# Kernel optimization log

Hardware: AMD Instinct MI355X
Metric: run time of the kernel (lower is better)

The kernel has to match this reference:

```python
import jax, jax.numpy as jnp
import numpy as np

B, T, D, H = 8, 1024, 512, 8
HD = D // H  # head_dim = 64


def conv1d(x, w, b):
    # x: [B, C_in, T], w: [C_out, C_in, 3], 'same' padding
    y = jax.lax.conv_general_dilated(x, w, (1,), [(1, 1)],
                                     dimension_numbers=('NCH', 'OIH', 'NCH'))
    return y + b[None, :, None]


def setup_inputs() -> dict:
    key = jax.random.key(0)
    ks = jax.random.split(key, 9)
    s = 0.05
    return {
        'x': jax.random.normal(ks[0], (B, T, D), dtype=jnp.float32),
        'w11': jax.random.normal(ks[1], (D, D, 3), dtype=jnp.float32) * s,
        'b11': jnp.zeros((D,), dtype=jnp.float32),
        'w12': jax.random.normal(ks[2], (D, D, 3), dtype=jnp.float32) * s,
        'b12': jnp.zeros((D,), dtype=jnp.float32),
        'w13': jax.random.normal(ks[3], (D, D, 3), dtype=jnp.float32) * s,
        'b13': jnp.zeros((D,), dtype=jnp.float32),
        'w2': jax.random.normal(ks[4], (D, 2 * D, 3), dtype=jnp.float32) * s,
        'b2': jnp.zeros((D,), dtype=jnp.float32),
    }


def reference(x, w11, b11, w12, b12, w13, b13, w2, b2):
    # dropout is identity in eval mode
    b, t, d = x.shape
    xc = jnp.transpose(x, (0, 2, 1))  # [B, D, T]

    def proj(w, bb):
        y = jax.nn.relu(conv1d(xc, w, bb))        # [B, D, T]
        y = jnp.transpose(y, (0, 2, 1))           # [B, T, D]
        return y.reshape(b, t, H, HD)             # [B, T, H, HD]

    q = proj(w11, b11)
    k = proj(w12, b12)
    v = proj(w13, b13)

    # ---- time-wise attention (d_k = head_dim) ----
    qf = jnp.transpose(q, (0, 2, 1, 3))  # [B, H, T, HD]
    kf = jnp.transpose(k, (0, 2, 1, 3))
    vf = jnp.transpose(v, (0, 2, 1, 3))
    sf = jnp.einsum('bhtd,bhsd->bhts', qf, kf) / np.sqrt(HD)  # [B,H,T,T]
    af = jax.nn.softmax(sf, axis=-1)
    valuesf = jnp.einsum('bhts,bhsd->bhtd', af, vf)           # [B,H,T,HD]
    valuesf = jnp.transpose(valuesf, (0, 2, 1, 3)).reshape(b, t, H * HD)

    # ---- channel-wise attention (d_k = T, scores over head_dim) ----
    qt = jnp.transpose(q, (0, 2, 3, 1))  # [B, H, HD, T]
    kt = jnp.transpose(k, (0, 2, 3, 1))
    vt = jnp.transpose(v, (0, 2, 3, 1))
    st = jnp.einsum('bhct,bhdt->bhcd', qt, kt) / np.sqrt(t)   # [B,H,HD,HD]
    at = jax.nn.softmax(st, axis=-1)
    valuest = jnp.einsum('bhcd,bhdt->bhct', at, vt)           # [B,H,HD,T]
    # torch: permute(0,2,3,1).reshape(B, T, H*HD)
    valuest = jnp.transpose(valuest, (0, 2, 3, 1)).reshape(b, t, H * HD)

    values = jnp.concatenate([valuesf, valuest], axis=-1)     # [B, T, 2D]
    values = jnp.transpose(values, (0, 2, 1))                 # [B, 2D, T]
    out = jax.nn.relu(conv1d(values, w2, b2))                 # [B, D, T]
    return jnp.transpose(out, (0, 2, 1))                      # [B, T, D]
```

## Files before the change

### kernel.cpp

```cpp
#include <hip/hip_runtime.h>

#define BB 8
#define TT 1024
#define DD 512
#define DD2 1024
#define HH 8
#define HDIM 64
#define TP (TT + 2)

typedef short short8 __attribute__((ext_vector_type(8)));
typedef float floatx4 __attribute__((ext_vector_type(4)));

typedef const __attribute__((address_space(1))) unsigned int* gas_ptr;
typedef __attribute__((address_space(3))) unsigned int* las_ptr;

__device__ __forceinline__ unsigned short f2bf(float f) {
    union { float f; unsigned u; } v; v.f = f;
    unsigned r = v.u + 0x7fffu + ((v.u >> 16) & 1u);
    return (unsigned short)(r >> 16);
}

__device__ __forceinline__ void gl2lds16(const void* g, void* l) {
    __builtin_amdgcn_global_load_lds((gas_ptr)g, (las_ptr)l, 16, 0, 0);
}

#define NX4BLK 4104
#define NW1BLK 9216
#define NW2BLK 6144
#define NZBLK 1024
__global__ void k_prep(const float* __restrict__ x, const float* __restrict__ w0,
                       const float* __restrict__ w1, const float* __restrict__ w2,
                       const float* __restrict__ wo,
                       unsigned short* __restrict__ xp, unsigned short* __restrict__ wqkv,
                       unsigned short* __restrict__ w2k, unsigned short* __restrict__ vp,
                       float* __restrict__ gbuf) {
    int blk = blockIdx.x;
    if (blk < NX4BLK) {
        int idx = blk * 256 + threadIdx.x;
        int c4 = idx % (DD / 4);
        int rt = idx / (DD / 4);
        int row = rt % TP;
        int b = rt / TP;
        ushort4 o = {0, 0, 0, 0};
        if (row >= 1 && row <= TT) {
            float4 vv = *(const float4*)&x[((size_t)(b * TT + row - 1)) * DD + c4 * 4];
            o.x = f2bf(vv.x); o.y = f2bf(vv.y); o.z = f2bf(vv.z); o.w = f2bf(vv.w);
        }
        *(ushort4*)&xp[(size_t)idx * 4] = o;
        return;
    }
    blk -= NX4BLK;
    if (blk < NW1BLK) {
        int idx = blk * 256 + threadIdx.x;
        int e = idx & 7;
        int lane = (idx >> 3) & 63;
        int co0 = (idx >> 9) & 31;
        int ci0 = (idx >> 14) & 15;
        int rest = idx >> 18;
        int k = rest % 3, p = rest / 3;
        int co = co0 * 16 + (lane & 15);
        int ci = ci0 * 32 + (lane >> 4) * 8 + e;
        const float* w = (p == 0) ? w0 : ((p == 1) ? w1 : w2);
        wqkv[idx] = f2bf(w[(co * DD + ci) * 3 + k]);
        return;
    }
    blk -= NW1BLK;
    if (blk < NW2BLK) {
        int idx = blk * 256 + threadIdx.x;
        int e = idx & 7;
        int lane = (idx >> 3) & 63;
        int co0 = (idx >> 9) & 31;
        int ci0 = (idx >> 14) & 31;
        int k = idx >> 19;
        int co = co0 * 16 + (lane & 15);
        int ci = ci0 * 32 + (lane >> 4) * 8 + e;
        w2k[idx] = f2bf(wo[(co * DD2 + ci) * 3 + k]);
        return;
    }
    blk -= NW2BLK;
    {
        int idx = blk * 256 + threadIdx.x;
        if (idx < BB * 2 * 2 * DD) {
            int c = idx % (2 * DD);
            int t1 = idx / (2 * DD);
            int row = (t1 & 1) ? (TT + 1) : 0;
            int b = t1 >> 1;
            vp[(b * TP + row) * (2 * DD) + c] = 0;
        }
        if (idx < 64 * HDIM * HDIM) gbuf[idx] = 0.f;
    }
}

__global__ __launch_bounds__(256) void k_qkv_conv(
    const unsigned short* __restrict__ xp, const unsigned short* __restrict__ wfrag,
    const float* __restrict__ b11, const float* __restrict__ b12, const float* __restrict__ b13,
    unsigned short* __restrict__ qt,
    unsigned short* __restrict__ kfrag, unsigned short* __restrict__ kt,
    unsigned short* __restrict__ v, unsigned short* __restrict__ vtfrag) {
    __shared__ short As[2][80 * 64];
    int wave = threadIdx.x >> 6, lane = threadIdx.x & 63;
    int l15 = lane & 15, quad = lane >> 4;
    int tb = blockIdx.x * 64;
    int cb = blockIdx.y * 128;
    int proj = blockIdx.z % 3, b = blockIdx.z / 3;
    const short* A = (const short*)xp + b * TP * DD;
    const short* WF = (const short*)wfrag + (size_t)proj * 786432 + lane * 8;
    int srow8 = lane >> 3;
    int scl = ((lane & 7) ^ srow8) * 8;
    int co0b = (cb >> 4) + wave * 2;

    floatx4 acc[4][2];
#pragma unroll
    for (int mi = 0; mi < 4; ++mi)
#pragma unroll
        for (int ni = 0; ni < 2; ++ni) acc[mi][ni] = (floatx4){0.f, 0.f, 0.f, 0.f};

    auto stage = [&](int it) {
        short* dst = As[it & 1];
        int cib = it * 64;
        for (int g = wave; g < 10; g += 4) {
            int j = g >> 1, hf = g & 1;
            int row = hf * 8 + srow8;
            gl2lds16(A + (tb + j * 16 + row) * DD + cib + scl, &dst[j * 1024 + hf * 512]);
        }
    };

    stage(0);
    __syncthreads();

    for (int it = 0; it < 8; ++it) {
        if (it < 7) stage(it + 1);
        const short* Asb = As[it & 1];
#pragma unroll
        for (int k = 0; k < 3; ++k) {
            short8 bf[2][2];
#pragma unroll
            for (int kf = 0; kf < 2; ++kf)
#pragma unroll
                for (int ni = 0; ni < 2; ++ni)
                    bf[kf][ni] = *(const short8*)(WF +
                        ((size_t)((k * 16 + it * 2 + kf) * 32 + co0b + ni) << 9));
#pragma unroll
            for (int kf = 0; kf < 2; ++kf) {
                short8 af[4];
#pragma unroll
                for (int mi = 0; mi < 4; ++mi) {
                    int arow = mi * 16 + l15 + k;
                    int cl = kf * 4 + quad;
                    af[mi] = *(const short8*)&Asb[arow * 64 + ((cl ^ (arow & 7)) << 3)];
                }
#pragma unroll
                for (int mi = 0; mi < 4; ++mi)
#pragma unroll
                    for (int ni = 0; ni < 2; ++ni)
                        acc[mi][ni] = __builtin_amdgcn_mfma_f32_16x16x32_bf16(af[mi], bf[kf][ni], acc[mi][ni], 0, 0, 0);
            }
        }
        __syncthreads();
    }

    const float* bias = (proj == 0) ? b11 : ((proj == 1) ? b12 : b13);
#pragma unroll
    for (int ni = 0; ni < 2; ++ni) {
        int co = cb + wave * 32 + ni * 16 + l15;
        float bv = bias[co];
        int h = co >> 6, hd = co & 63;
        int bh = b * HH + h;
#pragma unroll
        for (int mi = 0; mi < 4; ++mi) {
            int tbase = tb + mi * 16 + quad * 4;
            unsigned short bb[4];
            ushort4 pk;
#pragma unroll
            for (int r = 0; r < 4; ++r) {
                float val = fmaxf(acc[mi][ni][r] + bv, 0.f);
                bb[r] = f2bf(val);
                ((unsigned short*)&pk)[r] = bb[r];
            }
            if (proj == 0) {
                *(ushort4*)&qt[((size_t)bh * HDIM + hd) * TT + tbase] = pk;
            } else if (proj == 1) {
                *(ushort4*)&kt[((size_t)bh * HDIM + hd) * TT + tbase] = pk;
                int sblk = tbase >> 6;
                int jr = (quad & 1) + 2 * (mi >> 1);
                int l15a_base = 4 * (quad >> 1) + 8 * (mi & 1);
                int kf = hd >> 5, quad_a = (hd >> 3) & 3, elem = hd & 7;
                size_t base = ((((size_t)bh * 16 + sblk) * 4 + jr) * 2 + kf) * 512 +
                              quad_a * 128 + elem;
#pragma unroll
                for (int r = 0; r < 4; ++r)
                    kfrag[base + (l15a_base + r) * 8] = bb[r];
            } else {
#pragma unroll
                for (int r = 0; r < 4; ++r)
                    v[((size_t)bh * TT + tbase + r) * HDIM + hd] = bb[r];
                int sblk = tbase >> 6;
                int df = hd >> 4, l15a = hd & 15;
                int kf = mi >> 1;
                int quad_a = 2 * (mi & 1) + (quad >> 1);
                int elem = (quad & 1) * 4;
                size_t base = ((((size_t)bh * 16 + sblk) * 4 + df) * 2 + kf) * 512 +
                              (quad_a * 16 + l15a) * 8 + elem;
                *(ushort4*)&vtfrag[base] = pk;
            }
        }
    }
}

__global__ __launch_bounds__(256) void k_attn_gram(
    const unsigned short* __restrict__ kfrag, const unsigned short* __restrict__ vtfrag,
    const unsigned short* __restrict__ qt, const unsigned short* __restrict__ kt,
    float* __restrict__ gbuf, unsigned short* __restrict__ vp) {
    __shared__ short kvs[2][8192];
    int wave = threadIdx.x >> 6, lane = threadIdx.x & 63;
    int l15 = lane & 15, quad = lane >> 4;
    int bh = blockIdx.y;

    if (blockIdx.x < 16) {
        int b = bh >> 3, h = bh & 7;
        int qr = blockIdx.x * 64 + wave * 16;
        const short* Qt = (const short*)qt + (size_t)bh * HDIM * TT;
        const short* KF = (const short*)kfrag + (size_t)bh * 16 * 8 * 512 + lane * 8;
        const short* VF = (const short*)vtfrag + (size_t)bh * 16 * 8 * 512 + lane * 8;

        short8 bq[2];
#pragma unroll
        for (int kf = 0; kf < 2; ++kf) {
            union { short8 s; short v[8]; } u;
#pragma unroll
            for (int e = 0; e < 8; ++e)
                u.v[e] = Qt[(size_t)(kf * 32 + quad * 8 + e) * TT + qr + l15];
            bq[kf] = u.s;
        }

        floatx4 o[4];
#pragma unroll
        for (int df = 0; df < 4; ++df) o[df] = (floatx4){0.f, 0.f, 0.f, 0.f};
        float lacc = 0.f;

        auto stagekv = [&](int s) {
            short* dst = kvs[s & 1];
            for (int f = wave; f < 8; f += 4) {
                gl2lds16(KF + s * 4096 + f * 512, &dst[f * 512]);
                gl2lds16(VF + s * 4096 + f * 512, &dst[4096 + f * 512]);
            }
        };

        stagekv(0);
        __syncthreads();

        for (int sblk = 0; sblk < 16; ++sblk) {
            if (sblk < 15) stagekv(sblk + 1);
            const short* kb = (const short*)&kvs[sblk & 1][0] + lane * 8;
            const short* vb = kb + 4096;
            floatx4 c[4];
#pragma unroll
            for (int jr = 0; jr < 4; ++jr) c[jr] = (floatx4){0.f, 0.f, 0.f, 0.f};
#pragma unroll
            for (int jr = 0; jr < 4; ++jr) {
#pragma unroll
                for (int kf = 0; kf < 2; ++kf) {
                    short8 ak = *(const short8*)(kb + (jr * 2 + kf) * 512);
                    c[jr] = __builtin_amdgcn_mfma_f32_16x16x32_bf16(ak, bq[kf], c[jr], 0, 0, 0);
                }
            }
            short8 pb[2];
#pragma unroll
            for (int kf = 0; kf < 2; ++kf) {
                union { short8 s; unsigned u[4]; } pk;
#pragma unroll
                for (int half = 0; half < 2; ++half) {
                    floatx4 cc = c[2 * kf + half];
                    float p0 = __expf(cc[0] * 0.125f);
                    float p1 = __expf(cc[1] * 0.125f);
                    float p2 = __expf(cc[2] * 0.125f);
                    float p3 = __expf(cc[3] * 0.125f);
                    lacc += (p0 + p1) + (p2 + p3);
                    pk.u[half * 2] =
                        __builtin_amdgcn_perm(__float_as_uint(p1), __float_as_uint(p0), 0x07060302u);
                    pk.u[half * 2 + 1] =
                        __builtin_amdgcn_perm(__float_as_uint(p3), __float_as_uint(p2), 0x07060302u);
                }
                pb[kf] = pk.s;
            }
#pragma unroll
            for (int df = 0; df < 4; ++df) {
#pragma unroll
                for (int kf = 0; kf < 2; ++kf) {
                    short8 av = *(const short8*)(vb + (df * 2 + kf) * 512);
                    o[df] = __builtin_amdgcn_mfma_f32_16x16x32_bf16(av, pb[kf], o[df], 0, 0, 0);
                }
            }
            __syncthreads();
        }

        lacc += __shfl_xor(lacc, 16);
        lacc += __shfl_xor(lacc, 32);
        float linv = 1.f / lacc;

        unsigned short* vrow = vp + (size_t)(b * TP + 1 + qr + l15) * (2 * DD) + h * 64;
#pragma unroll
        for (int df = 0; df < 4; ++df) {
            ushort4 pk;
#pragma unroll
            for (int r = 0; r < 4; ++r) ((unsigned short*)&pk)[r] = f2bf(o[df][r] * linv);
            *(ushort4*)&vrow[df * 16 + quad * 4] = pk;
        }
    } else {
        int tc = blockIdx.x - 16;
        const short* Qt = (const short*)qt + (size_t)bh * HDIM * TT;
        const short* Kt = (const short*)kt + (size_t)bh * HDIM * TT;

        floatx4 g[4];
#pragma unroll
        for (int nt = 0; nt < 4; ++nt) g[nt] = (floatx4){0.f, 0.f, 0.f, 0.f};

        int t0b = tc * 256;
        for (int t0 = 0; t0 < 256; t0 += 32) {
            short8 aq = *(const short8*)(Qt + (wave * 16 + l15) * TT + t0b + t0 + quad * 8);
#pragma unroll
            for (int nt = 0; nt < 4; ++nt) {
                short8 bk = *(const short8*)(Kt + (nt * 16 + l15) * TT + t0b + t0 + quad * 8);
                g[nt] = __builtin_amdgcn_mfma_f32_16x16x32_bf16(aq, bk, g[nt], 0, 0, 0);
            }
        }
        float* gb = gbuf + bh * HDIM * HDIM;
#pragma unroll
        for (int nt = 0; nt < 4; ++nt) {
#pragma unroll
            for (int r = 0; r < 4; ++r) {
                int row = wave * 16 + quad * 4 + r;
                atomicAdd(&gb[row * HDIM + nt * 16 + l15], g[nt][r]);
            }
        }
    }
}

__global__ __launch_bounds__(256) void k_chan_av(
    const float* __restrict__ gbuf, const unsigned short* __restrict__ v,
    unsigned short* __restrict__ vp) {
    __shared__ short lds_a[64 * 64];
    int wave = threadIdx.x >> 6, lane = threadIdx.x & 63;
    int l15 = lane & 15, quad = lane >> 4;
    int tc = blockIdx.x, bh = blockIdx.y;
    int b = bh >> 3, h = bh & 7;
    const float sc = 0.03125f;

    if (threadIdx.x < 64) {
        const float* gb = gbuf + bh * HDIM * HDIM + threadIdx.x * HDIM;
        float mx = -3.0e38f;
        for (int j = 0; j < 64; ++j) mx = fmaxf(mx, gb[j] * sc);
        float sum = 0.f;
        for (int j = 0; j < 64; ++j) sum += __expf(gb[j] * sc - mx);
        float inv = 1.f / sum;
        for (int j = 0; j < 64; ++j)
            lds_a[threadIdx.x * 64 + j] = (short)f2bf(__expf(gb[j] * sc - mx) * inv);
    }
    __syncthreads();

    const short* V = (const short*)v + (size_t)bh * TT * HDIM;
    short8 pa[2];
#pragma unroll
    for (int kf = 0; kf < 2; ++kf)
        pa[kf] = *(const short8*)&lds_a[(wave * 16 + l15) * 64 + kf * 32 + quad * 8];

    for (int tt = 0; tt < 16; ++tt) {
        int ttile = tc * 16 + tt;
        floatx4 c = (floatx4){0.f, 0.f, 0.f, 0.f};
#pragma unroll
        for (int kf = 0; kf < 2; ++kf) {
            short8 bv = *(const short8*)(V + (ttile * 16 + l15) * HDIM + kf * 32 + quad * 8);
            c = __builtin_amdgcn_mfma_f32_16x16x32_bf16(pa[kf], bv, c, 0, 0, 0);
        }
        int t = ttile * 16 + l15;
#pragma unroll
        for (int r = 0; r < 4; ++r) {
            int crow = wave * 16 + quad * 4 + r;
            int tout = crow * 16 + (t >> 6);
            int col = 512 + ((t & 63) << 3) + h;
            vp[(b * TP + 1 + tout) * (2 * DD) + col] = f2bf(c[r]);
        }
    }
}

__global__ __launch_bounds__(256) void k_out_conv(
    const unsigned short* __restrict__ vp, const unsigned short* __restrict__ w2k,
    const float* __restrict__ b2, float* __restrict__ out) {
    __shared__ short As[2][144 * 64];
    int wave = threadIdx.x >> 6, lane = threadIdx.x & 63;
    int l15 = lane & 15, quad = lane >> 4;
    int wm = wave >> 1, wn = wave & 1;
    int tb = blockIdx.x * 128;
    int cb = blockIdx.y * 64;
    int b = blockIdx.z;
    const short* A = (const short*)vp + b * TP * DD2;
    const short* WF = (const short*)w2k + lane * 8;
    int srow8 = lane >> 3;
    int scl = ((lane & 7) ^ srow8) * 8;
    int co0b = (cb >> 4) + wn * 2;

    floatx4 acc[4][2];
#pragma unroll
    for (int mi = 0; mi < 4; ++mi)
#pragma unroll
        for (int ni = 0; ni < 2; ++ni) acc[mi][ni] = (floatx4){0.f, 0.f, 0.f, 0.f};

    auto stage = [&](int it) {
        short* dst = As[it & 1];
        int cib = it * 64;
        for (int g = wave; g < 18; g += 4) {
            int j = g >> 1, hf = g & 1;
            int row = hf * 8 + srow8;
            gl2lds16(A + (tb + j * 16 + row) * DD2 + cib + scl, &dst[j * 1024 + hf * 512]);
        }
    };

    stage(0);
    __syncthreads();

    for (int it = 0; it < 16; ++it) {
        if (it < 15) stage(it + 1);
        const short* Asb = As[it & 1];
#pragma unroll
        for (int k = 0; k < 3; ++k) {
            short8 bf[2][2];
#pragma unroll
            for (int kfh = 0; kfh < 2; ++kfh)
#pragma unroll
                for (int ni = 0; ni < 2; ++ni)
                    bf[kfh][ni] = *(const short8*)(WF +
                        ((size_t)((k * 32 + it * 2 + kfh) * 32 + co0b + ni) << 9));
#pragma unroll
            for (int kfh = 0; kfh < 2; ++kfh) {
                short8 af[4];
#pragma unroll
                for (int mi = 0; mi < 4; ++mi) {
                    int arow = wm * 64 + mi * 16 + l15 + k;
                    int cl = kfh * 4 + quad;
                    af[mi] = *(const short8*)&Asb[arow * 64 + ((cl ^ (arow & 7)) << 3)];
                }
#pragma unroll
                for (int mi = 0; mi < 4; ++mi)
#pragma unroll
                    for (int ni = 0; ni < 2; ++ni)
                        acc[mi][ni] = __builtin_amdgcn_mfma_f32_16x16x32_bf16(af[mi], bf[kfh][ni], acc[mi][ni], 0, 0, 0);
            }
        }
        __syncthreads();
    }

#pragma unroll
    for (int ni = 0; ni < 2; ++ni) {
        int co = cb + wn * 32 + ni * 16 + l15;
        float bv = b2[co];
#pragma unroll
        for (int mi = 0; mi < 4; ++mi) {
#pragma unroll
            for (int r = 0; r < 4; ++r) {
                int t = tb + wm * 64 + mi * 16 + quad * 4 + r;
                out[((size_t)b * TT + t) * DD + co] = fmaxf(acc[mi][ni][r] + bv, 0.f);
            }
        }
    }
}

extern "C" void kernel_launch(void* const* d_in, const int* in_sizes, int n_in,
                              void* d_out, int out_size, void* d_ws, size_t ws_size,
                              hipStream_t stream) {
    const float* x = (const float*)d_in[0];
    const float* w11 = (const float*)d_in[1];
    const float* b11 = (const float*)d_in[2];
    const float* w12 = (const float*)d_in[3];
    const float* b12 = (const float*)d_in[4];
    const float* w13 = (const float*)d_in[5];
    const float* b13 = (const float*)d_in[6];
    const float* w2 = (const float*)d_in[7];
    const float* b2 = (const float*)d_in[8];
    float* out = (float*)d_out;

    char* ws = (char*)d_ws;
    size_t off = 0;
    auto alloc = [&](size_t bytes) {
        void* p = ws + off;
        off += (bytes + 255) & ~(size_t)255;
        return p;
    };
    unsigned short* xp = (unsigned short*)alloc((size_t)BB * TP * DD * 2);
    unsigned short* wqkv = (unsigned short*)alloc((size_t)9 * DD * DD * 2);
    unsigned short* w2k = (unsigned short*)alloc((size_t)3 * DD * DD2 * 2);
    unsigned short* qt = (unsigned short*)alloc((size_t)BB * HH * TT * HDIM * 2);
    unsigned short* kfrag = (unsigned short*)alloc((size_t)BB * HH * TT * HDIM * 2);
    unsigned short* kt = (unsigned short*)alloc((size_t)BB * HH * TT * HDIM * 2);
    unsigned short* v = (unsigned short*)alloc((size_t)BB * HH * TT * HDIM * 2);
    unsigned short* vtfrag = (unsigned short*)alloc((size_t)BB * HH * TT * HDIM * 2);
    float* gbuf = (float*)alloc((size_t)64 * HDIM * HDIM * 4);
    unsigned short* vp = (unsigned short*)alloc((size_t)BB * TP * 2 * DD * 2);
    (void)alloc(65536);

    k_prep<<<NX4BLK + NW1BLK + NW2BLK + NZBLK, 256, 0, stream>>>(x, w11, w12, w13, w2,
                                                                 xp, wqkv, w2k, vp, gbuf);
    k_qkv_conv<<<dim3(TT / 64, DD / 128, BB * 3), 256, 0, stream>>>(xp, wqkv, b11, b12, b13,
                                                                    qt, kfrag, kt, v, vtfrag);
    k_attn_gram<<<dim3(20, BB * HH), 256, 0, stream>>>(kfrag, vtfrag, qt, kt, gbuf, vp);
    k_chan_av<<<dim3(4, BB * HH), 256, 0, stream>>>(gbuf, v, vp);
    k_out_conv<<<dim3(TT / 128, DD / 64, BB), 256, 0, stream>>>(vp, w2k, b2, out);
}
```

Baseline: 224.5 us.

## Restructure channel AV kernel to gather all heads per batch and coalesce stores

The channel-attention AV kernel now assigns one block per batch and time chunk covering all 8 heads, instead of one block per batch-head. Results go through an LDS staging tile so each output row segment of vp is written with contiguous 16-byte stores, where before each 2-byte store was strided by head. The cost is that every block recomputes the softmax for all 8 heads, adding redundant exp work. It also adds two block barriers per time tile and larger LDS use.

```diff
diff --git a/kernel.cpp b/kernel.cpp
--- a/kernel.cpp
+++ b/kernel.cpp
@@ -339,47 +339,67 @@
 __global__ __launch_bounds__(256) void k_chan_av(
     const float* __restrict__ gbuf, const unsigned short* __restrict__ v,
     unsigned short* __restrict__ vp) {
-    __shared__ short lds_a[64 * 64];
+    __shared__ short lds_a[8 * 64 * 64];
+    __shared__ short stg[64 * 128];
     int wave = threadIdx.x >> 6, lane = threadIdx.x & 63;
     int l15 = lane & 15, quad = lane >> 4;
-    int tc = blockIdx.x, bh = blockIdx.y;
-    int b = bh >> 3, h = bh & 7;
+    int tc = blockIdx.x, b = blockIdx.y;
     const float sc = 0.03125f;
 
-    if (threadIdx.x < 64) {
-        const float* gb = gbuf + bh * HDIM * HDIM + threadIdx.x * HDIM;
+    for (int p = threadIdx.x; p < 512; p += 256) {
+        int h = p >> 6, row = p & 63;
+        const float* gb = gbuf + (size_t)((b * 8 + h) * 64 + row) * 64;
         float mx = -3.0e38f;
-        for (int j = 0; j < 64; ++j) mx = fmaxf(mx, gb[j] * sc);
+        for (int j = 0; j < 16; ++j) {
+            float4 vv = *(const float4*)&gb[j * 4];
+            mx = fmaxf(mx, fmaxf(fmaxf(vv.x, vv.y), fmaxf(vv.z, vv.w)));
+        }
+        mx *= sc;
         float sum = 0.f;
         for (int j = 0; j < 64; ++j) sum += __expf(gb[j] * sc - mx);
         float inv = 1.f / sum;
         for (int j = 0; j < 64; ++j)
-            lds_a[threadIdx.x * 64 + j] = (short)f2bf(__expf(gb[j] * sc - mx) * inv);
+            lds_a[(h * 64 + row) * 64 + j] = (short)f2bf(__expf(gb[j] * sc - mx) * inv);
     }
     __syncthreads();
 
-    const short* V = (const short*)v + (size_t)bh * TT * HDIM;
-    short8 pa[2];
-#pragma unroll
-    for (int kf = 0; kf < 2; ++kf)
-        pa[kf] = *(const short8*)&lds_a[(wave * 16 + l15) * 64 + kf * 32 + quad * 8];
-
-    for (int tt = 0; tt < 16; ++tt) {
-        int ttile = tc * 16 + tt;
-        floatx4 c = (floatx4){0.f, 0.f, 0.f, 0.f};
-#pragma unroll
-        for (int kf = 0; kf < 2; ++kf) {
-            short8 bv = *(const short8*)(V + (ttile * 16 + l15) * HDIM + kf * 32 + quad * 8);
-            c = __builtin_amdgcn_mfma_f32_16x16x32_bf16(pa[kf], bv, c, 0, 0, 0);
-        }
-        int t = ttile * 16 + l15;
-#pragma unroll
-        for (int r = 0; r < 4; ++r) {
-            int crow = wave * 16 + quad * 4 + r;
-            int tout = crow * 16 + (t >> 6);
-            int col = 512 + ((t & 63) << 3) + h;
-            vp[(b * TP + 1 + tout) * (2 * DD) + col] = f2bf(c[r]);
-        }
+    for (int tt = 0; tt < 2; ++tt) {
+        int ttile = tc * 2 + tt;
+#pragma unroll
+        for (int hh = 0; hh < 2; ++hh) {
+            int h = wave * 2 + hh;
+            const short* V = (const short*)v + (size_t)(b * 8 + h) * TT * HDIM;
+            short8 bv[2];
+#pragma unroll
+            for (int kf = 0; kf < 2; ++kf)
+                bv[kf] = *(const short8*)(V + (ttile * 16 + l15) * HDIM + kf * 32 + quad * 8);
+#pragma unroll
+            for (int g = 0; g < 4; ++g) {
+                floatx4 c = (floatx4){0.f, 0.f, 0.f, 0.f};
+#pragma unroll
+                for (int kf = 0; kf < 2; ++kf) {
+                    short8 pa = *(const short8*)&lds_a[(h * 64 + g * 16 + l15) * 64 + kf * 32 + quad * 8];
+                    c = __builtin_amdgcn_mfma_f32_16x16x32_bf16(pa, bv[kf], c, 0, 0, 0);
+                }
+#pragma unroll
+                for (int r = 0; r < 4; ++r) {
+                    int crow = g * 16 + quad * 4 + r;
+                    stg[crow * 128 + l15 * 8 + h] = (short)f2bf(c[r]);
+                }
+            }
+        }
+        __syncthreads();
+        {
+            int row = threadIdx.x >> 2, chunk = threadIdx.x & 3;
+            int tout = row * 16 + (ttile >> 2);
+            unsigned short* dst = vp + (size_t)(b * TP + 1 + tout) * (2 * DD) + 512 +
+                                  (ttile & 3) * 128 + chunk * 32;
+            const short* src = &stg[row * 128 + chunk * 32];
+#pragma unroll
+            for (int e = 0; e < 4; ++e)
+                *(short8*)&dst[e * 8] = *(const short8*)&src[e * 8];
+        }
+        __syncthreads();
     }
 }
 
@@ -502,6 +522,6 @@
     k_qkv_conv<<<dim3(TT / 64, DD / 128, BB * 3), 256, 0, stream>>>(xp, wqkv, b11, b12, b13,
                                                                     qt, kfrag, kt, v, vtfrag);
     k_attn_gram<<<dim3(20, BB * HH), 256, 0, stream>>>(kfrag, vtfrag, qt, kt, gbuf, vp);
-    k_chan_av<<<dim3(4, BB * HH), 256, 0, stream>>>(gbuf, v, vp);
+    k_chan_av<<<dim3(32, BB), 256, 0, stream>>>(gbuf, v, vp);
     k_out_conv<<<dim3(TT / 128, DD / 64, BB), 256, 0, stream>>>(vp, w2k, b2, out);
 }
```

After: 226.5 us. No clear change (+0.9%).
